# Kernel optimization log

Measured on AMD Instinct MI355X. Metric: run time of the kernel, lower is better.

The kernel has to match this reference:

```python
import jax, jax.numpy as jnp
import numpy as np

N_USERS = 50000
N_ENTITIES = 50000
N_NODES = N_USERS + N_ENTITIES
CHANNEL = 128
N_HOPS = 2
N_HEADS = 2
N_RELATIONS = 16   # weight has n_relations-1 = 15 rows
N_PREFERS = 8
N_EDGES = 1000000
N_EXTRA_EDGES = 1000000
NNZ = 1000000


def _xavier(key, shape):
    a = np.sqrt(6.0 / (shape[0] + shape[1])).astype(np.float32)
    return jax.random.uniform(key, shape, jnp.float32, -a, a)


def setup_inputs() -> dict:
    key = jax.random.key(0)
    ks = jax.random.split(key, 13)
    user_emb = jax.random.normal(ks[0], (N_USERS, CHANNEL), jnp.float32) * 0.1
    entity_emb = jax.random.normal(ks[1], (N_ENTITIES, CHANNEL), jnp.float32) * 0.1
    edge_index = jax.random.randint(ks[2], (2, N_EDGES), 0, N_ENTITIES, jnp.int32)
    edge_type = jax.random.randint(ks[3], (N_EDGES,), 1, N_RELATIONS, jnp.int32)  # [1, 15]
    extra_edge_index = jax.random.randint(ks[4], (2, N_EXTRA_EDGES), 0, N_NODES, jnp.int32)
    extra_edge_type = jax.random.randint(ks[5], (N_EXTRA_EDGES,), 0, N_PREFERS, jnp.int32)
    interact_rows = jax.random.randint(ks[6], (NNZ,), 0, N_USERS, jnp.int32)
    interact_cols = jax.random.randint(ks[7], (NNZ,), 0, N_ENTITIES, jnp.int32)
    interact_vals = jax.random.uniform(ks[8], (NNZ,), jnp.float32)
    weight = _xavier(ks[9], (N_RELATIONS - 1, CHANNEL))
    extra_weight = _xavier(ks[10], (N_PREFERS, CHANNEL))
    W_Q = _xavier(ks[11], (CHANNEL, CHANNEL))
    W_K = _xavier(ks[12], (CHANNEL, CHANNEL))
    return {"user_emb": user_emb, "entity_emb": entity_emb, "edge_index": edge_index,
            "edge_type": edge_type, "extra_edge_index": extra_edge_index,
            "extra_edge_type": extra_edge_type, "interact_rows": interact_rows,
            "interact_cols": interact_cols, "interact_vals": interact_vals,
            "weight": weight, "extra_weight": extra_weight, "W_Q": W_Q, "W_K": W_K}


def _scatter_mean(src, index, dim_size):
    s = jax.ops.segment_sum(src, index, num_segments=dim_size)
    cnt = jax.ops.segment_sum(jnp.ones(src.shape[0], src.dtype), index, num_segments=dim_size)
    return s / jnp.maximum(cnt, 1.0)[:, None]


def _l2norm(x, eps=1e-12):
    n = jnp.sqrt(jnp.sum(x * x, axis=1, keepdims=True))
    return x / jnp.maximum(n, eps)


def _calc_attn_score(node_emb, head, tail, W_Q, W_K, n_nodes):
    # 2-head scaled dot-product attention with scatter-softmax over head node groups
    E = head.shape[0]
    d_k = node_emb.shape[1] // N_HEADS
    q = (node_emb[head] @ W_Q).reshape(E, N_HEADS, d_k)
    k = (node_emb[tail] @ W_K).reshape(E, N_HEADS, d_k)
    score = jnp.sum(q * k, axis=-1) / jnp.sqrt(jnp.asarray(d_k, node_emb.dtype))  # [E, H]
    m = jax.ops.segment_max(score, head, num_segments=n_nodes)  # [N, H]
    e = jnp.exp(score - m[head])
    z = jax.ops.segment_sum(e, head, num_segments=n_nodes)
    attn = e / z[head]
    return jnp.mean(attn, axis=1)  # [E]


def reference(user_emb, entity_emb, edge_index, edge_type, extra_edge_index,
              extra_edge_type, interact_rows, interact_cols, interact_vals,
              weight, extra_weight, W_Q, W_K):
    n_users, n_entities = user_emb.shape[0], entity_emb.shape[0]
    n_nodes = n_users + n_entities
    node_emb = jnp.concatenate([user_emb, entity_emb], axis=0)
    ent_head, ent_tail = edge_index[0], edge_index[1]
    ex_head, ex_tail = extra_edge_index[0], extra_edge_index[1]
    aug_w = _calc_attn_score(node_emb, ex_head, ex_tail, W_Q, W_K, n_nodes)[:, None]
    rel = edge_type - 1
    entity_res, node_res, user_res = entity_emb, node_emb, user_emb
    for _ in range(N_HOPS):
        # entity KG aggregation: gather tail, relation-embedding multiply, scatter-mean
        neigh = entity_emb[ent_tail] * weight[rel]
        entity_emb = _scatter_mean(neigh, ent_head, n_entities)
        # preference-graph aggregation (with_relation=False, attention edge weights)
        node_emb = _scatter_mean(node_emb[ex_tail] * aug_w, ex_head, n_nodes)
        # sparse interact_mat @ entity_emb
        user_emb = jax.ops.segment_sum(interact_vals[:, None] * entity_emb[interact_cols],
                                       interact_rows, num_segments=n_users)
        entity_emb = _l2norm(entity_emb)
        node_emb = _l2norm(node_emb)
        user_emb = _l2norm(user_emb)
        entity_res = entity_res + entity_emb
        node_res = node_res + node_emb
        user_res = user_res + user_emb
    gcn_res_emb = jnp.concatenate([user_res, entity_res], axis=0)
    return gcn_res_emb, node_res
```

## Files before the change

kernel.cpp:

```cpp
#include <hip/hip_runtime.h>
#include <math.h>

#define CH 128
#define SCAN_TILE 2048

__device__ __forceinline__ unsigned int bf16enc1(float f) {
  unsigned int b = __float_as_uint(f);
  return (b + 0x7fffu + ((b >> 16) & 1u)) >> 16;
}
__device__ __forceinline__ unsigned int bf16pack2(float lo, float hi) {
  return bf16enc1(lo) | (bf16enc1(hi) << 16);
}
__device__ __forceinline__ float bf16lo(unsigned int u) { return __uint_as_float(u << 16); }
__device__ __forceinline__ float bf16hi(unsigned int u) { return __uint_as_float(u & 0xffff0000u); }


__global__ void count_kernel(const int* __restrict__ dst, int n, int* __restrict__ cnt) {
  int stride = gridDim.x * blockDim.x;
  for (int e = blockIdx.x * blockDim.x + threadIdx.x; e < n; e += stride)
    atomicAdd(&cnt[dst[e]], 1);
}

__global__ __launch_bounds__(256) void scan_sum_kernel(const int* __restrict__ cnt, int n,
                                                       int* __restrict__ bsum) {
  __shared__ int red[4];
  int base = blockIdx.x * SCAN_TILE;
  int t = threadIdx.x;
  int idx = base + t * 8;
  int s = 0;
  if (idx + 8 <= n) {
    int4 a = *(const int4*)(cnt + idx);
    int4 b = *(const int4*)(cnt + idx + 4);
    s = a.x + a.y + a.z + a.w + b.x + b.y + b.z + b.w;
  } else {
    for (int i = 0; i < 8 && idx + i < n; ++i) s += cnt[idx + i];
  }
#pragma unroll
  for (int d = 32; d; d >>= 1) s += __shfl_xor(s, d);
  if ((t & 63) == 0) red[t >> 6] = s;
  __syncthreads();
  if (t == 0) bsum[blockIdx.x] = red[0] + red[1] + red[2] + red[3];
}

__global__ __launch_bounds__(64) void scan_mid_kernel(int* __restrict__ bsum, int n_tiles,
                                                      int* __restrict__ off, int n) {
  int lane = threadIdx.x;
  int v = (lane < n_tiles) ? bsum[lane] : 0;
  int x = v;
#pragma unroll
  for (int d = 1; d < 64; d <<= 1) {
    int t = __shfl_up(x, d);
    if (lane >= d) x += t;
  }
  if (lane < n_tiles) bsum[lane] = x - v;
  if (lane == 63) off[n] = x;
}

__global__ __launch_bounds__(256) void scan_apply_kernel(const int* __restrict__ cnt, int n,
                                                         const int* __restrict__ bsum,
                                                         int* __restrict__ off) {
  __shared__ int wsums[4];
  int base = blockIdx.x * SCAN_TILE;
  int t = threadIdx.x;
  int idx = base + t * 8;
  int v[8];
  int s = 0;
  if (idx + 8 <= n) {
    int4 a = *(const int4*)(cnt + idx);
    int4 b = *(const int4*)(cnt + idx + 4);
    v[0] = a.x; v[1] = a.y; v[2] = a.z; v[3] = a.w;
    v[4] = b.x; v[5] = b.y; v[6] = b.z; v[7] = b.w;
    s = v[0] + v[1] + v[2] + v[3] + v[4] + v[5] + v[6] + v[7];
  } else {
#pragma unroll
    for (int i = 0; i < 8; ++i) {
      int j = idx + i;
      v[i] = (j < n) ? cnt[j] : 0;
      s += v[i];
    }
  }
  int lane = t & 63, wid = t >> 6;
  int x = s;
#pragma unroll
  for (int d = 1; d < 64; d <<= 1) {
    int tt = __shfl_up(x, d);
    if (lane >= d) x += tt;
  }
  if (lane == 63) wsums[wid] = x;
  __syncthreads();
  int wbase = 0;
  if (wid > 0) wbase += wsums[0];
  if (wid > 1) wbase += wsums[1];
  if (wid > 2) wbase += wsums[2];
  int run = bsum[blockIdx.x] + wbase + (x - s);
#pragma unroll
  for (int i = 0; i < 8; ++i) {
    int j = idx + i;
    if (j < n) off[j] = run;
    run += v[i];
  }
}

__global__ void fill_kg_kernel(const int* __restrict__ head, const int* __restrict__ tail,
                               const int* __restrict__ type, int n,
                               const int* __restrict__ off, int* __restrict__ cur,
                               int2* __restrict__ pay) {
  int stride = gridDim.x * blockDim.x;
  for (int e = blockIdx.x * blockDim.x + threadIdx.x; e < n; e += stride) {
    int d = head[e];
    int p = off[d] + atomicAdd(&cur[d], 1);
    pay[p] = make_int2(tail[e], type[e] - 1);
  }
}

__global__ void fill_ex_kernel(const int* __restrict__ head, const int* __restrict__ tail,
                               int n, const int* __restrict__ off, int* __restrict__ cur,
                               int* __restrict__ pay , int* __restrict__ slot) {
  int stride = gridDim.x * blockDim.x;
  for (int e = blockIdx.x * blockDim.x + threadIdx.x; e < n; e += stride) {
    int d = head[e];
    int p = off[d] + atomicAdd(&cur[d], 1);
    pay[2 * (size_t)p] = tail[e];
    slot[e] = p;
  }
}

__global__ void fill_it_kernel(const int* __restrict__ rows, const int* __restrict__ cols,
                               const float* __restrict__ vals, int n,
                               const int* __restrict__ off, int* __restrict__ cur,
                               int2* __restrict__ pay) {
  int stride = gridDim.x * blockDim.x;
  for (int e = blockIdx.x * blockDim.x + threadIdx.x; e < n; e += stride) {
    int d = rows[e];
    int p = off[d] + atomicAdd(&cur[d], 1);
    pay[p] = make_int2(cols[e], __float_as_int(vals[e]));
  }
}

__global__ void init_out_kernel(const float* __restrict__ user, const float* __restrict__ ent,
                                float* __restrict__ out, int nu4, int ne4) {
  int i = blockIdx.x * blockDim.x + threadIdx.x;
  int half = nu4 + ne4;
  if (i >= 2 * half) return;
  int k = (i >= half) ? i - half : i;
  float4 v = (k < nu4) ? ((const float4*)user)[k] : ((const float4*)ent)[k - nu4];
  ((float4*)out)[i] = v;
}

__global__ __launch_bounds__(256) void qk_kernel(const float* __restrict__ user,
                                                 const float* __restrict__ ent,
                                                 const float* __restrict__ Wmat,
                                                 unsigned short* __restrict__ Out,
                                                 int n_users, int n_nodes) {
  __shared__ float X[32 * CH];
  const int t = threadIdx.x;
  const int row0 = blockIdx.x * 32;
  for (int i = t; i < 32 * 32; i += 256) {
    int r = i >> 5, c4 = i & 31;
    int row = row0 + r;
    float4 v = make_float4(0.f, 0.f, 0.f, 0.f);
    if (row < n_nodes) {
      const float* src = (row < n_users) ? (user + (size_t)row * CH)
                                         : (ent + (size_t)(row - n_users) * CH);
      v = ((const float4*)src)[c4];
    }
    ((float4*)X)[i] = v;
  }
  __syncthreads();
  const int c = t & 127;
  const int rg = t >> 7;
  float acc[16];
#pragma unroll
  for (int r = 0; r < 16; ++r) acc[r] = 0.f;
  for (int k4 = 0; k4 < CH; k4 += 4) {
    float w0 = Wmat[(k4 + 0) * CH + c];
    float w1 = Wmat[(k4 + 1) * CH + c];
    float w2 = Wmat[(k4 + 2) * CH + c];
    float w3 = Wmat[(k4 + 3) * CH + c];
#pragma unroll
    for (int r = 0; r < 16; ++r) {
      float4 x = *(const float4*)&X[(rg * 16 + r) * CH + k4];
      acc[r] += x.x * w0 + x.y * w1 + x.z * w2 + x.w * w3;
    }
  }
  for (int r = 0; r < 16; ++r) {
    int row = row0 + rg * 16 + r;
    if (row < n_nodes) Out[(size_t)row * CH + c] = (unsigned short)bf16enc1(acc[r]);
  }
}

__global__ __launch_bounds__(256) void escore_kernel(const uint4* __restrict__ Q,
                                                     const uint4* __restrict__ K,
                                                     const int* __restrict__ eh,
                                                     const int* __restrict__ et,
                                                     const int* __restrict__ slot,
                                                     float2* __restrict__ scores, int n_edges) {
  int g = (int)((blockIdx.x * 256 + threadIdx.x) >> 4);
  int gl = threadIdx.x & 15;
  if (g >= n_edges) return;
  int h = eh[g], tl = et[g];
  uint4 qu = Q[(size_t)h * 16 + gl];
  uint4 ku = K[(size_t)tl * 16 + gl];
  float p = bf16lo(qu.x) * bf16lo(ku.x) + bf16hi(qu.x) * bf16hi(ku.x);
  p += bf16lo(qu.y) * bf16lo(ku.y) + bf16hi(qu.y) * bf16hi(ku.y);
  p += bf16lo(qu.z) * bf16lo(ku.z) + bf16hi(qu.z) * bf16hi(ku.z);
  p += bf16lo(qu.w) * bf16lo(ku.w) + bf16hi(qu.w) * bf16hi(ku.w);
#pragma unroll
  for (int d = 1; d < 8; d <<= 1) p += __shfl_xor(p, d);
  float p1 = __shfl_xor(p, 8);
  if (gl == 0) scores[slot[g]] = make_float2(p * 0.125f, p1 * 0.125f);
}

__global__ __launch_bounds__(256) void attn_kernel(const int* __restrict__ off,
                                                   const float2* __restrict__ scores,
                                                   int* __restrict__ pay_ex ,
                                                   int n_nodes) {
  int wid = (int)((blockIdx.x * 256 + threadIdx.x) >> 6);
  int lane = threadIdx.x & 63;
  if (wid >= n_nodes) return;
  int o0 = off[wid], o1 = off[wid + 1];
  int deg = o1 - o0;
  if (deg == 0) return;
  float m0 = -3.4e38f, m1 = -3.4e38f;
  for (int i = lane; i < deg; i += 64) {
    float2 s = scores[o0 + i];
    m0 = fmaxf(m0, s.x);
    m1 = fmaxf(m1, s.y);
  }
#pragma unroll
  for (int d = 32; d; d >>= 1) {
    m0 = fmaxf(m0, __shfl_xor(m0, d));
    m1 = fmaxf(m1, __shfl_xor(m1, d));
  }
  float z0 = 0.f, z1 = 0.f;
  for (int i = lane; i < deg; i += 64) {
    float2 s = scores[o0 + i];
    z0 += expf(s.x - m0);
    z1 += expf(s.y - m1);
  }
#pragma unroll
  for (int d = 32; d; d >>= 1) {
    z0 += __shfl_xor(z0, d);
    z1 += __shfl_xor(z1, d);
  }
  float iz0 = 1.f / z0, iz1 = 1.f / z1;
  for (int i = lane; i < deg; i += 64) {
    float2 s = scores[o0 + i];
    float a = 0.5f * (expf(s.x - m0) * iz0 + expf(s.y - m1) * iz1);
    pay_ex[2 * (size_t)(o0 + i) + 1] = __float_as_int(a);
  }
}


template <int HOP2>
__global__ __launch_bounds__(256) void entity_agg_kernel(
    const float* __restrict__ src, const int2* __restrict__ pay,
    const float* __restrict__ weight, const int* __restrict__ off,
    const float* __restrict__ rscale_in, float* __restrict__ Eout,
    float* __restrict__ rscale_out, float* __restrict__ res, int n) {
  int w = (int)((blockIdx.x * 256 + threadIdx.x) >> 5);
  int lane = threadIdx.x & 31;
  if (w >= n) return;
  int o0 = off[w], o1 = off[w + 1];
  float a0 = 0.f, a1 = 0.f, a2 = 0.f, a3 = 0.f;
#define EBODY(I)                                                      \
  {                                                                   \
    int2 pr = pay[I];                                                 \
    float rs = HOP2 ? rscale_in[pr.x] : 1.f;                          \
    float4 sv = ((const float4*)(src + (size_t)pr.x * CH))[lane];     \
    float4 wv = ((const float4*)(weight + (size_t)pr.y * CH))[lane];  \
    a0 += sv.x * wv.x * rs;                                           \
    a1 += sv.y * wv.y * rs;                                           \
    a2 += sv.z * wv.z * rs;                                           \
    a3 += sv.w * wv.w * rs;                                           \
  }
  int i = o0;
  for (; i + 4 <= o1; i += 4) { EBODY(i) EBODY(i + 1) EBODY(i + 2) EBODY(i + 3) }
  for (; i < o1; ++i) EBODY(i)
#undef EBODY
  int deg = o1 - o0;
  float inv = 1.f / (float)(deg > 0 ? deg : 1);
  a0 *= inv; a1 *= inv; a2 *= inv; a3 *= inv;
  float ss = a0 * a0 + a1 * a1 + a2 * a2 + a3 * a3;
#pragma unroll
  for (int d = 16; d; d >>= 1) ss += __shfl_xor(ss, d);
  float scale = 1.f / fmaxf(sqrtf(ss), 1e-12f);
  ((float4*)(Eout + (size_t)w * CH))[lane] = make_float4(a0, a1, a2, a3);
  if (!HOP2 && lane == 0) rscale_out[w] = scale;
  float4* rp = (float4*)(res + (size_t)w * CH);
  float4 r = rp[lane];
  r.x += a0 * scale; r.y += a1 * scale; r.z += a2 * scale; r.w += a3 * scale;
  rp[lane] = r;
}

template <int BF>
__global__ __launch_bounds__(256) void node_agg_kernel(
    const void* __restrict__ srcU, const void* __restrict__ srcE,
    const int2* __restrict__ pay, const int* __restrict__ off,
    uint2* __restrict__ Nout ,
    float* __restrict__ res, int n, int n_users, int write_norm) {
  int w = (int)((blockIdx.x * 256 + threadIdx.x) >> 5);
  int lane = threadIdx.x & 31;
  if (w >= n) return;
  int o0 = off[w], o1 = off[w + 1];
  float a0 = 0.f, a1 = 0.f, a2 = 0.f, a3 = 0.f;
#define NBODY(I)                                                          \
  {                                                                       \
    int2 pr = pay[I];                                                     \
    float aw = __int_as_float(pr.y);                                      \
    int tl = pr.x;                                                        \
    int r_ = (tl < n_users) ? tl : tl - n_users;                          \
    if (BF) {                                                             \
      const uint2* b = (const uint2*)((tl < n_users) ? srcU : srcE);      \
      uint2 u = b[(size_t)r_ * 32 + lane];                                \
      a0 += bf16lo(u.x) * aw;                                             \
      a1 += bf16hi(u.x) * aw;                                             \
      a2 += bf16lo(u.y) * aw;                                             \
      a3 += bf16hi(u.y) * aw;                                             \
    } else {                                                              \
      const float* b = (const float*)((tl < n_users) ? srcU : srcE);      \
      float4 sv = ((const float4*)(b + (size_t)r_ * CH))[lane];           \
      a0 += sv.x * aw; a1 += sv.y * aw; a2 += sv.z * aw; a3 += sv.w * aw; \
    }                                                                     \
  }
  int i = o0;
  for (; i + 4 <= o1; i += 4) { NBODY(i) NBODY(i + 1) NBODY(i + 2) NBODY(i + 3) }
  for (; i < o1; ++i) NBODY(i)
#undef NBODY
  int deg = o1 - o0;
  float inv = 1.f / (float)(deg > 0 ? deg : 1);
  a0 *= inv; a1 *= inv; a2 *= inv; a3 *= inv;
  float ss = a0 * a0 + a1 * a1 + a2 * a2 + a3 * a3;
#pragma unroll
  for (int d = 16; d; d >>= 1) ss += __shfl_xor(ss, d);
  float scale = 1.f / fmaxf(sqrtf(ss), 1e-12f);
  float n0 = a0 * scale, n1 = a1 * scale, n2 = a2 * scale, n3 = a3 * scale;
  if (write_norm)
    Nout[(size_t)w * 32 + lane] = make_uint2(bf16pack2(n0, n1), bf16pack2(n2, n3));
  float4* rp = (float4*)(res + (size_t)w * CH);
  float4 r = rp[lane];
  r.x += n0; r.y += n1; r.z += n2; r.w += n3;
  rp[lane] = r;
}

__global__ __launch_bounds__(256) void user_agg_kernel(const float* __restrict__ Eun,
                                                       const int2* __restrict__ pay,
                                                       const int* __restrict__ off,
                                                       float* __restrict__ res, int n) {
  int w = (int)((blockIdx.x * 256 + threadIdx.x) >> 5);
  int lane = threadIdx.x & 31;
  if (w >= n) return;
  int o0 = off[w], o1 = off[w + 1];
  float a0 = 0.f, a1 = 0.f, a2 = 0.f, a3 = 0.f;
#define UBODY(I)                                                    \
  {                                                                 \
    int2 pr = pay[I];                                               \
    float v = __int_as_float(pr.y);                                 \
    float4 sv = ((const float4*)(Eun + (size_t)pr.x * CH))[lane];   \
    a0 += sv.x * v; a1 += sv.y * v; a2 += sv.z * v; a3 += sv.w * v; \
  }
  int i = o0;
  for (; i + 4 <= o1; i += 4) { UBODY(i) UBODY(i + 1) UBODY(i + 2) UBODY(i + 3) }
  for (; i < o1; ++i) UBODY(i)
#undef UBODY
  float ss = a0 * a0 + a1 * a1 + a2 * a2 + a3 * a3;
#pragma unroll
  for (int d = 16; d; d >>= 1) ss += __shfl_xor(ss, d);
  float scale = 1.f / fmaxf(sqrtf(ss), 1e-12f);
  float4* rp = (float4*)(res + (size_t)w * CH);
  float4 r = rp[lane];
  r.x += a0 * scale; r.y += a1 * scale; r.z += a2 * scale; r.w += a3 * scale;
  rp[lane] = r;
}


extern "C" void kernel_launch(void* const* d_in, const int* in_sizes, int n_in,
                              void* d_out, int out_size, void* d_ws, size_t ws_size,
                              hipStream_t stream) {
  const float* user_emb = (const float*)d_in[0];
  const float* ent_emb  = (const float*)d_in[1];
  const int*   edge_index = (const int*)d_in[2];
  const int*   edge_type  = (const int*)d_in[3];
  const int*   ex_index   = (const int*)d_in[4];
  const int*   it_rows = (const int*)d_in[6];
  const int*   it_cols = (const int*)d_in[7];
  const float* it_vals = (const float*)d_in[8];
  const float* weight  = (const float*)d_in[9];
  const float* W_Q = (const float*)d_in[11];
  const float* W_K = (const float*)d_in[12];

  const int n_users = in_sizes[0] / CH;
  const int n_ents  = in_sizes[1] / CH;
  const int n_nodes = n_users + n_ents;
  const int n_kg    = in_sizes[3];
  const int n_ex    = in_sizes[5];
  const int nnz     = in_sizes[8];

  const int* kg_head = edge_index;
  const int* kg_tail = edge_index + n_kg;
  const int* ex_head = ex_index;
  const int* ex_tail = ex_index + n_ex;

  char* p = (char*)d_ws;
  auto alloc = [&](size_t bytes) -> char* {
    char* r = p;
    p += (bytes + 255) & ~(size_t)255;
    return r;
  };
  int2* pay_kg = (int2*)alloc((size_t)n_kg * 8);
  int2* pay_ex = (int2*)alloc((size_t)n_ex * 8);
  size_t slotb = ((size_t)n_ex * 4 + 255) & ~(size_t)255;
  size_t unionA = slotb + (size_t)n_ex * 8;
  size_t unionB = (size_t)nnz * 8;
  char* uA = alloc(unionA > unionB ? unionA : unionB);
  int*    slot_ex = (int*)uA;
  float2* scores  = (float2*)(uA + slotb);
  int2*   pay_it  = (int2*)uA;
  char* cnt_base = alloc((size_t)(n_ents + n_nodes + n_users) * 4);
  int* cnt_kg = (int*)cnt_base;
  int* cnt_ex = cnt_kg + n_ents;
  int* cnt_it = cnt_ex + n_nodes;
  size_t cnt_bytes = (size_t)(n_ents + n_nodes + n_users) * 4;
  int* off_kg = (int*)alloc((size_t)(n_ents + 1) * 4);
  int* off_ex = (int*)alloc((size_t)(n_nodes + 1) * 4);
  int* off_it = (int*)alloc((size_t)(n_users + 1) * 4);
  int* bsum_kg = (int*)alloc(64 * 4);
  int* bsum_ex = (int*)alloc(64 * 4);
  int* bsum_it = (int*)alloc(64 * 4);
  size_t arenaA = (size_t)2 * n_nodes * CH * 2;
  size_t arenaB = (size_t)2 * n_ents * CH * 4 + (size_t)n_ents * 4 + 256 +
                  (size_t)n_nodes * CH * 2;
  char* arena = alloc(arenaA > arenaB ? arenaA : arenaB);
  unsigned int* Qbf = (unsigned int*)arena;
  unsigned int* Kbf = Qbf + (size_t)n_nodes * 64;
  float* EunA = (float*)arena;
  float* EunB = EunA + (size_t)n_ents * CH;
  float* rscaleE = EunB + (size_t)n_ents * CH;
  uint2* Nnbf = (uint2*)(((uintptr_t)(rscaleE + n_ents) + 255) & ~(uintptr_t)255);

  float* res_user = (float*)d_out;
  float* res_ent  = (float*)d_out + (size_t)n_users * CH;
  float* res_node = (float*)d_out + (size_t)n_nodes * CH;

  const int t_kg = (n_ents + SCAN_TILE - 1) / SCAN_TILE;
  const int t_ex = (n_nodes + SCAN_TILE - 1) / SCAN_TILE;
  const int t_it = (n_users + SCAN_TILE - 1) / SCAN_TILE;

  hipMemsetAsync(cnt_base, 0, cnt_bytes, stream);
  count_kernel<<<2048, 256, 0, stream>>>(kg_head, n_kg, cnt_kg);
  count_kernel<<<2048, 256, 0, stream>>>(ex_head, n_ex, cnt_ex);
  count_kernel<<<2048, 256, 0, stream>>>(it_rows, nnz, cnt_it);
  scan_sum_kernel<<<t_kg, 256, 0, stream>>>(cnt_kg, n_ents, bsum_kg);
  scan_sum_kernel<<<t_ex, 256, 0, stream>>>(cnt_ex, n_nodes, bsum_ex);
  scan_sum_kernel<<<t_it, 256, 0, stream>>>(cnt_it, n_users, bsum_it);
  scan_mid_kernel<<<1, 64, 0, stream>>>(bsum_kg, t_kg, off_kg, n_ents);
  scan_mid_kernel<<<1, 64, 0, stream>>>(bsum_ex, t_ex, off_ex, n_nodes);
  scan_mid_kernel<<<1, 64, 0, stream>>>(bsum_it, t_it, off_it, n_users);
  scan_apply_kernel<<<t_kg, 256, 0, stream>>>(cnt_kg, n_ents, bsum_kg, off_kg);
  scan_apply_kernel<<<t_ex, 256, 0, stream>>>(cnt_ex, n_nodes, bsum_ex, off_ex);
  scan_apply_kernel<<<t_it, 256, 0, stream>>>(cnt_it, n_users, bsum_it, off_it);
  hipMemsetAsync(cnt_base, 0, cnt_bytes, stream);
  fill_kg_kernel<<<2048, 256, 0, stream>>>(kg_head, kg_tail, edge_type, n_kg, off_kg,
                                           cnt_kg, pay_kg);
  fill_ex_kernel<<<2048, 256, 0, stream>>>(ex_head, ex_tail, n_ex, off_ex, cnt_ex,
                                           (int*)pay_ex, slot_ex);

  {
    int nu4 = n_users * (CH / 4), ne4 = n_ents * (CH / 4);
    int total = 2 * (nu4 + ne4);
    init_out_kernel<<<(total + 255) / 256, 256, 0, stream>>>(user_emb, ent_emb,
                                                             (float*)d_out, nu4, ne4);
  }

  {
    int blocks = (n_nodes + 31) / 32;
    qk_kernel<<<blocks, 256, 0, stream>>>(user_emb, ent_emb, W_Q, (unsigned short*)Qbf,
                                          n_users, n_nodes);
    qk_kernel<<<blocks, 256, 0, stream>>>(user_emb, ent_emb, W_K, (unsigned short*)Kbf,
                                          n_users, n_nodes);
  }
  escore_kernel<<<(n_ex + 15) / 16, 256, 0, stream>>>((const uint4*)Qbf, (const uint4*)Kbf,
                                                      ex_head, ex_tail, slot_ex, scores,
                                                      n_ex);
  attn_kernel<<<(n_nodes + 3) / 4, 256, 0, stream>>>(off_ex, scores, (int*)pay_ex, n_nodes);

  fill_it_kernel<<<2048, 256, 0, stream>>>(it_rows, it_cols, it_vals, nnz, off_it, cnt_it,
                                           pay_it);

  entity_agg_kernel<0><<<(n_ents + 7) / 8, 256, 0, stream>>>(
      ent_emb, pay_kg, weight, off_kg, nullptr, EunA, rscaleE, res_ent, n_ents);
  node_agg_kernel<0><<<(n_nodes + 7) / 8, 256, 0, stream>>>(
      user_emb, ent_emb, pay_ex, off_ex, Nnbf, res_node, n_nodes, n_users, 1);
  user_agg_kernel<<<(n_users + 7) / 8, 256, 0, stream>>>(EunA, pay_it, off_it, res_user,
                                                         n_users);

  entity_agg_kernel<1><<<(n_ents + 7) / 8, 256, 0, stream>>>(
      EunA, pay_kg, weight, off_kg, rscaleE, EunB, nullptr, res_ent, n_ents);
  node_agg_kernel<1><<<(n_nodes + 7) / 8, 256, 0, stream>>>(
      Nnbf, Nnbf + (size_t)n_users * 32, pay_ex, off_ex, Nnbf, res_node, n_nodes,
      n_users, 0);
  user_agg_kernel<<<(n_users + 7) / 8, 256, 0, stream>>>(EunB, pay_it, off_it, res_user,
                                                         n_users);
}
```

Measured before the change: 1.215 ms.

## Use bf16 MFMA for fused Q/K projection and reuse bf16 embeddings in hop one

Replaces the two scalar FP32 Q and K projection kernels with a single MFMA kernel. It works on bf16 copies of the inputs and of pre-transposed weights, and computes Q and K from one shared tile load. The same kernel also writes a bf16 copy of the node embeddings, which hop-one entity and node aggregation then gather instead of FP32 rows, halving gather bandwidth. The cost is bf16 rounding of the hop-one inputs and an extra workspace region, with a fallback to the old FP32 path when the workspace is too small.

```diff
diff --git a/kernel.cpp b/kernel.cpp
--- a/kernel.cpp
+++ b/kernel.cpp
@@ -3,6 +3,9 @@
 
 #define CH 128
 #define SCAN_TILE 2048
+
+typedef __attribute__((ext_vector_type(8))) short short8v;
+typedef __attribute__((ext_vector_type(4))) float float4v;
 
 __device__ __forceinline__ unsigned int bf16enc1(float f) {
   unsigned int b = __float_as_uint(f);
@@ -147,45 +150,66 @@
   ((float4*)out)[i] = v;
 }
 
-__global__ __launch_bounds__(256) void qk_kernel(const float* __restrict__ user,
-                                                 const float* __restrict__ ent,
-                                                 const float* __restrict__ Wmat,
-                                                 unsigned short* __restrict__ Out,
-                                                 int n_users, int n_nodes) {
-  __shared__ float X[32 * CH];
+__global__ __launch_bounds__(256) void wtrans_kernel(const float* __restrict__ WQ,
+                                                     const float* __restrict__ WK,
+                                                     unsigned short* __restrict__ WtQ,
+                                                     unsigned short* __restrict__ WtK) {
+  int idx = blockIdx.x * 256 + threadIdx.x;
+  if (idx >= CH * CH) return;
+  int k = idx >> 7, c = idx & 127;
+  WtQ[c * CH + k] = (unsigned short)bf16enc1(WQ[idx]);
+  WtK[c * CH + k] = (unsigned short)bf16enc1(WK[idx]);
+}
+
+__global__ __launch_bounds__(256) void qk_mfma_kernel(
+    const float* __restrict__ user, const float* __restrict__ ent,
+    const unsigned short* __restrict__ WtQ, const unsigned short* __restrict__ WtK,
+    unsigned short* __restrict__ OutQ, unsigned short* __restrict__ OutK,
+    unsigned int* __restrict__ Xnbf, int n_users, int n_nodes) {
+  __shared__ unsigned short Xb[64 * 136];
   const int t = threadIdx.x;
-  const int row0 = blockIdx.x * 32;
-  for (int i = t; i < 32 * 32; i += 256) {
-    int r = i >> 5, c4 = i & 31;
+  const int row0 = blockIdx.x * 64;
+  for (int u = t; u < 64 * 64; u += 256) {
+    int r = u >> 6, c2 = u & 63;
     int row = row0 + r;
-    float4 v = make_float4(0.f, 0.f, 0.f, 0.f);
+    float2 v = make_float2(0.f, 0.f);
     if (row < n_nodes) {
       const float* src = (row < n_users) ? (user + (size_t)row * CH)
                                          : (ent + (size_t)(row - n_users) * CH);
-      v = ((const float4*)src)[c4];
+      v = ((const float2*)src)[c2];
     }
-    ((float4*)X)[i] = v;
+    unsigned int pk = bf16pack2(v.x, v.y);
+    *(unsigned int*)&Xb[r * 136 + c2 * 2] = pk;
+    if (Xnbf != nullptr && row < n_nodes) Xnbf[(size_t)row * 64 + c2] = pk;
   }
   __syncthreads();
-  const int c = t & 127;
-  const int rg = t >> 7;
-  float acc[16];
-#pragma unroll
-  for (int r = 0; r < 16; ++r) acc[r] = 0.f;
-  for (int k4 = 0; k4 < CH; k4 += 4) {
-    float w0 = Wmat[(k4 + 0) * CH + c];
-    float w1 = Wmat[(k4 + 1) * CH + c];
-    float w2 = Wmat[(k4 + 2) * CH + c];
-    float w3 = Wmat[(k4 + 3) * CH + c];
-#pragma unroll
-    for (int r = 0; r < 16; ++r) {
-      float4 x = *(const float4*)&X[(rg * 16 + r) * CH + k4];
-      acc[r] += x.x * w0 + x.y * w1 + x.z * w2 + x.w * w3;
+  const int w = t >> 6;
+  const int l = t & 63;
+  const int rl = (w << 4) + (l & 15);
+  const int lg = l >> 4;
+  short8v a[4];
+#pragma unroll
+  for (int kk = 0; kk < 4; ++kk)
+    a[kk] = *(const short8v*)&Xb[rl * 136 + kk * 32 + lg * 8];
+#pragma unroll
+  for (int tb = 0; tb < 2; ++tb) {
+    const unsigned short* W = tb ? WtK : WtQ;
+    unsigned short* O = tb ? OutK : OutQ;
+#pragma unroll
+    for (int ct = 0; ct < 8; ++ct) {
+      float4v acc = {0.f, 0.f, 0.f, 0.f};
+#pragma unroll
+      for (int kk = 0; kk < 4; ++kk) {
+        short8v b = *(const short8v*)&W[(ct * 16 + (l & 15)) * CH + kk * 32 + lg * 8];
+        acc = __builtin_amdgcn_mfma_f32_16x16x32_bf16(a[kk], b, acc, 0, 0, 0);
+      }
+      int col = ct * 16 + (l & 15);
+#pragma unroll
+      for (int i = 0; i < 4; ++i) {
+        int row = row0 + (w << 4) + lg * 4 + i;
+        if (row < n_nodes) O[(size_t)row * CH + col] = (unsigned short)bf16enc1(acc[i]);
+      }
     }
-  }
-  for (int r = 0; r < 16; ++r) {
-    int row = row0 + rg * 16 + r;
-    if (row < n_nodes) Out[(size_t)row * CH + c] = (unsigned short)bf16enc1(acc[r]);
   }
 }
 
@@ -213,7 +237,7 @@
 
 __global__ __launch_bounds__(256) void attn_kernel(const int* __restrict__ off,
                                                    const float2* __restrict__ scores,
-                                                   int* __restrict__ pay_ex ,
+                                                   int* __restrict__ pay_ex,
                                                    int n_nodes) {
   int wid = (int)((blockIdx.x * 256 + threadIdx.x) >> 6);
   int lane = threadIdx.x & 63;
@@ -252,9 +276,9 @@
 }
 
 
-template <int HOP2>
+template <int HOP2, int BF>
 __global__ __launch_bounds__(256) void entity_agg_kernel(
-    const float* __restrict__ src, const int2* __restrict__ pay,
+    const void* __restrict__ src, const int2* __restrict__ pay,
     const float* __restrict__ weight, const int* __restrict__ off,
     const float* __restrict__ rscale_in, float* __restrict__ Eout,
     float* __restrict__ rscale_out, float* __restrict__ res, int n) {
@@ -263,16 +287,23 @@
   if (w >= n) return;
   int o0 = off[w], o1 = off[w + 1];
   float a0 = 0.f, a1 = 0.f, a2 = 0.f, a3 = 0.f;
-#define EBODY(I)                                                      \
-  {                                                                   \
-    int2 pr = pay[I];                                                 \
-    float rs = HOP2 ? rscale_in[pr.x] : 1.f;                          \
-    float4 sv = ((const float4*)(src + (size_t)pr.x * CH))[lane];     \
-    float4 wv = ((const float4*)(weight + (size_t)pr.y * CH))[lane];  \
-    a0 += sv.x * wv.x * rs;                                           \
-    a1 += sv.y * wv.y * rs;                                           \
-    a2 += sv.z * wv.z * rs;                                           \
-    a3 += sv.w * wv.w * rs;                                           \
+#define EBODY(I)                                                            \
+  {                                                                         \
+    int2 pr = pay[I];                                                       \
+    float rs = HOP2 ? rscale_in[pr.x] : 1.f;                                \
+    float4 wv = ((const float4*)(weight + (size_t)pr.y * CH))[lane];        \
+    float sx, sy, sz, sw;                                                   \
+    if (BF) {                                                               \
+      uint2 u = ((const uint2*)src)[(size_t)pr.x * 32 + lane];              \
+      sx = bf16lo(u.x); sy = bf16hi(u.x); sz = bf16lo(u.y); sw = bf16hi(u.y); \
+    } else {                                                                \
+      float4 sv = ((const float4*)src)[(size_t)pr.x * 32 + lane];           \
+      sx = sv.x; sy = sv.y; sz = sv.z; sw = sv.w;                           \
+    }                                                                       \
+    a0 += sx * wv.x * rs;                                                   \
+    a1 += sy * wv.y * rs;                                                   \
+    a2 += sz * wv.z * rs;                                                   \
+    a3 += sw * wv.w * rs;                                                   \
   }
   int i = o0;
   for (; i + 4 <= o1; i += 4) { EBODY(i) EBODY(i + 1) EBODY(i + 2) EBODY(i + 3) }
@@ -297,8 +328,8 @@
 __global__ __launch_bounds__(256) void node_agg_kernel(
     const void* __restrict__ srcU, const void* __restrict__ srcE,
     const int2* __restrict__ pay, const int* __restrict__ off,
-    uint2* __restrict__ Nout ,
-    float* __restrict__ res, int n, int n_users, int write_norm) {
+    uint2* __restrict__ Nout, float* __restrict__ res, int n, int n_users,
+    int write_norm) {
   int w = (int)((blockIdx.x * 256 + threadIdx.x) >> 5);
   int lane = threadIdx.x & 31;
   if (w >= n) return;
@@ -427,16 +458,24 @@
   int* bsum_kg = (int*)alloc(64 * 4);
   int* bsum_ex = (int*)alloc(64 * 4);
   int* bsum_it = (int*)alloc(64 * 4);
-  size_t arenaA = (size_t)2 * n_nodes * CH * 2;
-  size_t arenaB = (size_t)2 * n_ents * CH * 4 + (size_t)n_ents * 4 + 256 +
-                  (size_t)n_nodes * CH * 2;
-  char* arena = alloc(arenaA > arenaB ? arenaA : arenaB);
+  unsigned short* WtQ = (unsigned short*)alloc((size_t)CH * CH * 2);
+  unsigned short* WtK = (unsigned short*)alloc((size_t)CH * CH * 2);
+
+  size_t sizeA = (size_t)2 * n_nodes * CH * 2;
+  size_t sizeB = (size_t)2 * n_ents * CH * 4 + (((size_t)n_ents * 4 + 255) & ~(size_t)255) +
+                 (size_t)n_nodes * CH * 2 + 512;
+  size_t region0 = ((sizeA > sizeB ? sizeA : sizeB) + 255) & ~(size_t)255;
+  size_t xbytes = (size_t)n_nodes * CH * 2;
+  size_t used = (size_t)(p - (char*)d_ws);
+  bool fitX = (used + region0 + xbytes + 4096) <= ws_size;
+  char* arena = alloc(region0 + (fitX ? xbytes : 0));
   unsigned int* Qbf = (unsigned int*)arena;
   unsigned int* Kbf = Qbf + (size_t)n_nodes * 64;
   float* EunA = (float*)arena;
   float* EunB = EunA + (size_t)n_ents * CH;
   float* rscaleE = EunB + (size_t)n_ents * CH;
   uint2* Nnbf = (uint2*)(((uintptr_t)(rscaleE + n_ents) + 255) & ~(uintptr_t)255);
+  unsigned int* Xnbf = fitX ? (unsigned int*)(arena + region0) : nullptr;
 
   float* res_user = (float*)d_out;
   float* res_ent  = (float*)d_out + (size_t)n_users * CH;
@@ -472,13 +511,10 @@
                                                              (float*)d_out, nu4, ne4);
   }
 
-  {
-    int blocks = (n_nodes + 31) / 32;
-    qk_kernel<<<blocks, 256, 0, stream>>>(user_emb, ent_emb, W_Q, (unsigned short*)Qbf,
-                                          n_users, n_nodes);
-    qk_kernel<<<blocks, 256, 0, stream>>>(user_emb, ent_emb, W_K, (unsigned short*)Kbf,
-                                          n_users, n_nodes);
-  }
+  wtrans_kernel<<<(CH * CH + 255) / 256, 256, 0, stream>>>(W_Q, W_K, WtQ, WtK);
+  qk_mfma_kernel<<<(n_nodes + 63) / 64, 256, 0, stream>>>(
+      user_emb, ent_emb, WtQ, WtK, (unsigned short*)Qbf, (unsigned short*)Kbf, Xnbf,
+      n_users, n_nodes);
   escore_kernel<<<(n_ex + 15) / 16, 256, 0, stream>>>((const uint4*)Qbf, (const uint4*)Kbf,
                                                       ex_head, ex_tail, slot_ex, scores,
                                                       n_ex);
@@ -487,14 +523,23 @@
   fill_it_kernel<<<2048, 256, 0, stream>>>(it_rows, it_cols, it_vals, nnz, off_it, cnt_it,
                                            pay_it);
 
-  entity_agg_kernel<0><<<(n_ents + 7) / 8, 256, 0, stream>>>(
-      ent_emb, pay_kg, weight, off_kg, nullptr, EunA, rscaleE, res_ent, n_ents);
-  node_agg_kernel<0><<<(n_nodes + 7) / 8, 256, 0, stream>>>(
-      user_emb, ent_emb, pay_ex, off_ex, Nnbf, res_node, n_nodes, n_users, 1);
+  if (Xnbf != nullptr) {
+    entity_agg_kernel<0, 1><<<(n_ents + 7) / 8, 256, 0, stream>>>(
+        (const uint2*)Xnbf + (size_t)n_users * 32, pay_kg, weight, off_kg, nullptr, EunA,
+        rscaleE, res_ent, n_ents);
+    node_agg_kernel<1><<<(n_nodes + 7) / 8, 256, 0, stream>>>(
+        Xnbf, (const uint2*)Xnbf + (size_t)n_users * 32, pay_ex, off_ex, Nnbf, res_node,
+        n_nodes, n_users, 1);
+  } else {
+    entity_agg_kernel<0, 0><<<(n_ents + 7) / 8, 256, 0, stream>>>(
+        ent_emb, pay_kg, weight, off_kg, nullptr, EunA, rscaleE, res_ent, n_ents);
+    node_agg_kernel<0><<<(n_nodes + 7) / 8, 256, 0, stream>>>(
+        user_emb, ent_emb, pay_ex, off_ex, Nnbf, res_node, n_nodes, n_users, 1);
+  }
   user_agg_kernel<<<(n_users + 7) / 8, 256, 0, stream>>>(EunA, pay_it, off_it, res_user,
                                                          n_users);
 
-  entity_agg_kernel<1><<<(n_ents + 7) / 8, 256, 0, stream>>>(
+  entity_agg_kernel<1, 0><<<(n_ents + 7) / 8, 256, 0, stream>>>(
       EunA, pay_kg, weight, off_kg, rscaleE, EunB, nullptr, res_ent, n_ents);
   node_agg_kernel<1><<<(n_nodes + 7) / 8, 256, 0, stream>>>(
       Nnbf, Nnbf + (size_t)n_users * 32, pay_ex, off_ex, Nnbf, res_node, n_nodes,
```

After: 1.072 ms. 11.7% less time.
